# Kernel tuning notes

Measured on AMD Instinct MI355X. Metric: run time of the kernel, lower is better.

The kernel has to match this reference:

```python
import jax, jax.numpy as jnp
import numpy as np

GROUP_SIZE = 64
IN_FEATURES = 4096
OUT_FEATURES = 4096
NUM_GROUPS = OUT_FEATURES * IN_FEATURES // GROUP_SIZE  # 262144
BYTES_PER_GROUP = GROUP_SIZE // 8 * 3  # 24
TOKENS = 8192


def block_dequantize_3bit(packed, scale, group_size=GROUP_SIZE):
    # packed: (G, bytes_per_group) int32 holding byte values 0..255
    p = packed.astype(jnp.uint8).astype(jnp.int32)  # byte semantics
    t = p.reshape(p.shape[0], -1, 3)  # (G, group_size//8, 3)
    b0, b1, b2 = t[..., 0], t[..., 1], t[..., 2]
    c0 = b0 & 7
    c1 = (b0 >> 3) & 7
    c2 = ((b0 >> 6) & 3) | ((b1 & 1) << 2)
    c3 = (b1 >> 1) & 7
    c4 = (b1 >> 4) & 7
    c5 = ((b1 >> 7) & 1) | ((b2 & 3) << 1)
    c6 = (b2 >> 2) & 7
    c7 = (b2 >> 5) & 7
    codes = jnp.stack([c0, c1, c2, c3, c4, c5, c6, c7], axis=-1)
    codes = codes.reshape(p.shape[0], group_size)  # (G, group_size)
    q = jnp.clip(codes - 3, -3, 3).astype(jnp.float32)
    return (q * scale.astype(jnp.float32)).reshape(-1)


def setup_inputs() -> dict:
    key = jax.random.key(0)
    k1, k2, k3, k4 = jax.random.split(key, 4)
    x = jax.random.normal(k1, (TOKENS, IN_FEATURES), dtype=jnp.float32)
    weight_q3 = jax.random.randint(k2, (NUM_GROUPS, BYTES_PER_GROUP), 0, 256, dtype=jnp.int32)
    weight_scale = jax.random.uniform(k3, (NUM_GROUPS, 1), dtype=jnp.float32)
    bias = jax.random.normal(k4, (OUT_FEATURES,), dtype=jnp.float32)
    return {"x": x, "weight_q3": weight_q3, "weight_scale": weight_scale, "bias": bias}


def reference(x, weight_q3, weight_scale, bias):
    w = block_dequantize_3bit(weight_q3, weight_scale).reshape(OUT_FEATURES, IN_FEATURES)
    out = jnp.einsum('ti,oi->to', x.astype(jnp.float32), w) + bias
    return out.astype(x.dtype)
```

## Files before the change

kernel.cpp:

```cpp
#include <hip/hip_runtime.h>

#define M_TOK 8192
#define N_OUT 4096
#define K_IN  4096
#define BK    64
#define NT    (K_IN / BK)

typedef __bf16 bf16;
typedef bf16  bf16x4  __attribute__((ext_vector_type(4)));
typedef bf16  bf16x8  __attribute__((ext_vector_type(8)));
typedef float floatx4 __attribute__((ext_vector_type(4)));

__device__ __forceinline__ bf16 dec_code(int c, float s) {
    int q = (c > 6 ? 6 : c) - 3;
    return (bf16)((float)q * s);
}

__device__ __forceinline__ void async_ld16(const bf16* g, const bf16* l) {
    __builtin_amdgcn_global_load_lds(
        (const __attribute__((address_space(1))) void*)g,
        (__attribute__((address_space(3))) void*)l,
        16, 0, 0);
}

__global__ __launch_bounds__(256)
void dequant_kernel(const int* __restrict__ wq, const float* __restrict__ wscale,
                    bf16* __restrict__ W)
{
    int idx  = blockIdx.x * 256 + threadIdx.x;
    int g    = idx >> 1;
    int half = idx & 1;
    const int* wp = wq + (size_t)g * 24 + half * 12;
    int4 r0 = *(const int4*)(wp);
    int4 r1 = *(const int4*)(wp + 4);
    int4 r2 = *(const int4*)(wp + 8);
    float s = wscale[g];
    int by[12] = { r0.x, r0.y, r0.z, r0.w, r1.x, r1.y, r1.z, r1.w,
                   r2.x, r2.y, r2.z, r2.w };
    bf16* dst = W + (size_t)g * 64 + half * 32;
#pragma unroll
    for (int tri = 0; tri < 4; ++tri) {
        int b0 = by[tri * 3 + 0];
        int b1 = by[tri * 3 + 1];
        int b2 = by[tri * 3 + 2];
        bf16x8 h;
        h[0] = dec_code(b0 & 7, s);
        h[1] = dec_code((b0 >> 3) & 7, s);
        h[2] = dec_code(((b0 >> 6) & 3) | ((b1 & 1) << 2), s);
        h[3] = dec_code((b1 >> 1) & 7, s);
        h[4] = dec_code((b1 >> 4) & 7, s);
        h[5] = dec_code(((b1 >> 7) & 1) | ((b2 & 3) << 1), s);
        h[6] = dec_code((b2 >> 2) & 7, s);
        h[7] = dec_code((b2 >> 5) & 7, s);
        *(bf16x8*)(dst + tri * 8) = h;
    }
}

__global__ __launch_bounds__(256)
void cvt_kernel(const float* __restrict__ x, bf16* __restrict__ xb)
{
    size_t i = ((size_t)blockIdx.x * 256 + threadIdx.x) * 8;
    float4 a = *(const float4*)(x + i);
    float4 b = *(const float4*)(x + i + 4);
    bf16x8 h = { (bf16)a.x, (bf16)a.y, (bf16)a.z, (bf16)a.w,
                 (bf16)b.x, (bf16)b.y, (bf16)b.z, (bf16)b.w };
    *(bf16x8*)(xb + i) = h;
}

__global__ __launch_bounds__(256, 2)
void gemm_kernel(const bf16* __restrict__ A, const bf16* __restrict__ B,
                 const float* __restrict__ bias, float* __restrict__ out)
{
    __shared__ bf16 As[128][BK];
    __shared__ bf16 Bs[128][BK];

    const int t     = threadIdx.x;
    const int nBase = blockIdx.x * 128;
    const int mBase = blockIdx.y * 128;

    const int wave = t >> 6;
    const int lane = t & 63;
    const int quad = lane >> 4;
    const int r16  = lane & 15;
    const int wm   = wave & 1;
    const int wn   = wave >> 1;

    const int rr  = lane >> 3;
    const int cc  = lane & 7;
    const int lch = cc ^ rr;

    const bf16* aBase = A + (size_t)(mBase + wave * 32 + rr) * K_IN + lch * 8;
    const bf16* bBase = B + (size_t)(nBase + wave * 32 + rr) * K_IN + lch * 8;
    const bf16* aLds  = &As[wave * 32][0] + lane * 8;
    const bf16* bLds  = &Bs[wave * 32][0] + lane * 8;

    floatx4 acc[4][4];
#pragma unroll
    for (int i = 0; i < 4; ++i)
#pragma unroll
        for (int j = 0; j < 4; ++j)
            acc[i][j] = (floatx4){0.f, 0.f, 0.f, 0.f};

    const int sw = r16 & 7;

    for (int kt = 0; kt < NT; ++kt) {
        __syncthreads();
#pragma unroll
        for (int j = 0; j < 4; ++j) {
            async_ld16(aBase + (size_t)j * 8 * K_IN + kt * BK, aLds + j * 8 * BK);
            async_ld16(bBase + (size_t)j * 8 * K_IN + kt * BK, bLds + j * 8 * BK);
        }
        __syncthreads();

#pragma unroll
        for (int ks = 0; ks < 2; ++ks) {
            bf16x8 af[4], bfr[4];
#pragma unroll
            for (int mi = 0; mi < 4; ++mi)
                af[mi] = *(const bf16x8*)(&As[wm * 64 + mi * 16 + r16]
                                            [((ks * 4 + quad) ^ sw) * 8]);
#pragma unroll
            for (int ni = 0; ni < 4; ++ni)
                bfr[ni] = *(const bf16x8*)(&Bs[wn * 64 + ni * 16 + r16]
                                             [((ks * 4 + quad) ^ sw) * 8]);
#pragma unroll
            for (int mi = 0; mi < 4; ++mi)
#pragma unroll
                for (int ni = 0; ni < 4; ++ni)
                    acc[mi][ni] = __builtin_amdgcn_mfma_f32_16x16x32_bf16(
                        af[mi], bfr[ni], acc[mi][ni], 0, 0, 0);
        }
    }

    const int colBase = nBase + wn * 64;
#pragma unroll
    for (int ni = 0; ni < 4; ++ni) {
        int col  = colBase + ni * 16 + r16;
        float bv = bias[col];
#pragma unroll
        for (int mi = 0; mi < 4; ++mi) {
            int row0 = mBase + wm * 64 + mi * 16 + quad * 4;
#pragma unroll
            for (int r = 0; r < 4; ++r)
                out[(size_t)(row0 + r) * N_OUT + col] = acc[mi][ni][r] + bv;
        }
    }
}

__global__ __launch_bounds__(256, 2)
void linear3bit_fused(const float* __restrict__ x,
                      const int*   __restrict__ wq,
                      const float* __restrict__ wscale,
                      const float* __restrict__ bias,
                      float*       __restrict__ out)
{
    __shared__ bf16 As[128][BK];
    __shared__ bf16 Bs[128][BK];

    const int t     = threadIdx.x;
    const int mBase = blockIdx.y * 128;
    const int nBase = blockIdx.x * 128;

    const int wave = t >> 6;
    const int lane = t & 63;
    const int quad = lane >> 4;
    const int r16  = lane & 15;
    const int wm   = wave & 1;
    const int wn   = wave >> 1;

    floatx4 acc[4][4];
#pragma unroll
    for (int i = 0; i < 4; ++i)
#pragma unroll
        for (int j = 0; j < 4; ++j)
            acc[i][j] = (floatx4){0.f, 0.f, 0.f, 0.f};

    const int gl   = t >> 1;
    const int half = t & 1;
    const float* xBase = x + (size_t)mBase * K_IN;

    float4 aReg[8];
    int4   bReg[3];
    float  sReg;

    auto loadTile = [&](int kt) {
#pragma unroll
        for (int i = 0; i < 8; ++i) {
            int linear = i * 256 + t;
            int row    = linear >> 4;
            int c4     = (linear & 15) << 2;
            aReg[i] = *(const float4*)(xBase + (size_t)row * K_IN + kt * BK + c4);
        }
        size_t g = (size_t)(nBase + gl) * 64 + kt;
        const int* wp = wq + g * 24 + half * 12;
        bReg[0] = *(const int4*)(wp);
        bReg[1] = *(const int4*)(wp + 4);
        bReg[2] = *(const int4*)(wp + 8);
        sReg = wscale[g];
    };

    auto stage = [&]() {
#pragma unroll
        for (int i = 0; i < 8; ++i) {
            int linear = i * 256 + t;
            int row    = linear >> 4;
            int c4     = (linear & 15) << 2;
            float4 v = aReg[i];
            bf16x4 h = { (bf16)v.x, (bf16)v.y, (bf16)v.z, (bf16)v.w };
            *(bf16x4*)(&As[row][c4]) = h;
        }
        const float s = sReg;
        int by[12] = { bReg[0].x, bReg[0].y, bReg[0].z, bReg[0].w,
                       bReg[1].x, bReg[1].y, bReg[1].z, bReg[1].w,
                       bReg[2].x, bReg[2].y, bReg[2].z, bReg[2].w };
#pragma unroll
        for (int tri = 0; tri < 4; ++tri) {
            int b0 = by[tri * 3 + 0];
            int b1 = by[tri * 3 + 1];
            int b2 = by[tri * 3 + 2];
            bf16x8 h;
            h[0] = dec_code(b0 & 7, s);
            h[1] = dec_code((b0 >> 3) & 7, s);
            h[2] = dec_code(((b0 >> 6) & 3) | ((b1 & 1) << 2), s);
            h[3] = dec_code((b1 >> 1) & 7, s);
            h[4] = dec_code((b1 >> 4) & 7, s);
            h[5] = dec_code(((b1 >> 7) & 1) | ((b2 & 3) << 1), s);
            h[6] = dec_code((b2 >> 2) & 7, s);
            h[7] = dec_code((b2 >> 5) & 7, s);
            *(bf16x8*)(&Bs[gl][half * 32 + tri * 8]) = h;
        }
    };

    auto compute = [&]() {
#pragma unroll
        for (int ks = 0; ks < 2; ++ks) {
            bf16x8 af[4], bfr[4];
#pragma unroll
            for (int mi = 0; mi < 4; ++mi)
                af[mi] = *(const bf16x8*)(&As[wm * 64 + mi * 16 + r16][ks * 32 + quad * 8]);
#pragma unroll
            for (int ni = 0; ni < 4; ++ni)
                bfr[ni] = *(const bf16x8*)(&Bs[wn * 64 + ni * 16 + r16][ks * 32 + quad * 8]);
#pragma unroll
            for (int mi = 0; mi < 4; ++mi)
#pragma unroll
                for (int ni = 0; ni < 4; ++ni)
                    acc[mi][ni] = __builtin_amdgcn_mfma_f32_16x16x32_bf16(
                        af[mi], bfr[ni], acc[mi][ni], 0, 0, 0);
        }
    };

    loadTile(0);
    for (int kt = 0; kt < NT; ++kt) {
        __syncthreads();
        stage();
        __syncthreads();
        if (kt + 1 < NT) loadTile(kt + 1);
        compute();
    }

    const int colBase = nBase + wn * 64;
#pragma unroll
    for (int ni = 0; ni < 4; ++ni) {
        int col  = colBase + ni * 16 + r16;
        float bv = bias[col];
#pragma unroll
        for (int mi = 0; mi < 4; ++mi) {
            int row0 = mBase + wm * 64 + mi * 16 + quad * 4;
#pragma unroll
            for (int r = 0; r < 4; ++r)
                out[(size_t)(row0 + r) * N_OUT + col] = acc[mi][ni][r] + bv;
        }
    }
}

extern "C" void kernel_launch(void* const* d_in, const int* in_sizes, int n_in,
                              void* d_out, int out_size, void* d_ws, size_t ws_size,
                              hipStream_t stream) {
    const float* x      = (const float*)d_in[0];
    const int*   wq     = (const int*)d_in[1];
    const float* wscale = (const float*)d_in[2];
    const float* bias   = (const float*)d_in[3];
    float*       out    = (float*)d_out;

    const size_t wBytes  = (size_t)N_OUT * K_IN * sizeof(bf16);
    const size_t xBytes  = (size_t)M_TOK * K_IN * sizeof(bf16);

    if (ws_size >= wBytes + xBytes) {
        bf16* Wb = (bf16*)d_ws;
        bf16* Xb = (bf16*)((char*)d_ws + wBytes);
        dequant_kernel<<<2048, 256, 0, stream>>>(wq, wscale, Wb);
        cvt_kernel<<<16384, 256, 0, stream>>>(x, Xb);
        dim3 grid(N_OUT / 128, M_TOK / 128);
        gemm_kernel<<<grid, dim3(256), 0, stream>>>(Xb, Wb, bias, out);
    } else {
        dim3 grid(N_OUT / 128, M_TOK / 128);
        linear3bit_fused<<<grid, dim3(256), 0, stream>>>(x, wq, wscale, bias, out);
    }
}
```

Baseline: 484.5 us.

## Pre-swizzle dequantized weights into MFMA fragment order and load B directly to registers

The dequant kernel now writes weights in a layout that matches the MFMA B-fragment order, so each lane of the GEMM can fetch its B operand with a contiguous 16-byte global load. The B tile no longer goes through LDS, and the next k-tile is prefetched into registers while the current one is consumed. The aim is to cut LDS traffic and occupancy pressure for B. In exchange, each wave fetches its B fragments from global or L2 separately, with no sharing through LDS, and register pressure rises from the doubled B buffers. The cvt kernel also handles 16 elements per thread.

```diff
diff --git a/kernel.cpp b/kernel.cpp
--- a/kernel.cpp
+++ b/kernel.cpp
@@ -25,11 +25,16 @@
 
 __global__ __launch_bounds__(256)
 void dequant_kernel(const int* __restrict__ wq, const float* __restrict__ wscale,
-                    bf16* __restrict__ W)
+                    bf16* __restrict__ Wsw)
 {
     int idx  = blockIdx.x * 256 + threadIdx.x;
     int g    = idx >> 1;
     int half = idx & 1;
+    int n    = g >> 6;
+    int kg   = g & 63;
+    int k0   = kg * 2 + half;
+    int n0   = n >> 4;
+    int r16  = n & 15;
     const int* wp = wq + (size_t)g * 24 + half * 12;
     int4 r0 = *(const int4*)(wp);
     int4 r1 = *(const int4*)(wp + 4);
@@ -37,7 +42,7 @@
     float s = wscale[g];
     int by[12] = { r0.x, r0.y, r0.z, r0.w, r1.x, r1.y, r1.z, r1.w,
                    r2.x, r2.y, r2.z, r2.w };
-    bf16* dst = W + (size_t)g * 64 + half * 32;
+    bf16* dst = Wsw + (((size_t)n0 * 128 + k0) * 64 + r16) * 8;
 #pragma unroll
     for (int tri = 0; tri < 4; ++tri) {
         int b0 = by[tri * 3 + 0];
@@ -52,27 +57,29 @@
         h[5] = dec_code(((b1 >> 7) & 1) | ((b2 & 3) << 1), s);
         h[6] = dec_code((b2 >> 2) & 7, s);
         h[7] = dec_code((b2 >> 5) & 7, s);
-        *(bf16x8*)(dst + tri * 8) = h;
+        *(bf16x8*)(dst + (size_t)tri * 16 * 8) = h;
     }
 }
 
 __global__ __launch_bounds__(256)
 void cvt_kernel(const float* __restrict__ x, bf16* __restrict__ xb)
 {
-    size_t i = ((size_t)blockIdx.x * 256 + threadIdx.x) * 8;
-    float4 a = *(const float4*)(x + i);
-    float4 b = *(const float4*)(x + i + 4);
-    bf16x8 h = { (bf16)a.x, (bf16)a.y, (bf16)a.z, (bf16)a.w,
-                 (bf16)b.x, (bf16)b.y, (bf16)b.z, (bf16)b.w };
-    *(bf16x8*)(xb + i) = h;
+    size_t i = ((size_t)blockIdx.x * 256 + threadIdx.x) * 16;
+#pragma unroll
+    for (int h = 0; h < 2; ++h) {
+        float4 a = *(const float4*)(x + i + h * 8);
+        float4 b = *(const float4*)(x + i + h * 8 + 4);
+        bf16x8 v = { (bf16)a.x, (bf16)a.y, (bf16)a.z, (bf16)a.w,
+                     (bf16)b.x, (bf16)b.y, (bf16)b.z, (bf16)b.w };
+        *(bf16x8*)(xb + i + h * 8) = v;
+    }
 }
 
 __global__ __launch_bounds__(256, 2)
-void gemm_kernel(const bf16* __restrict__ A, const bf16* __restrict__ B,
+void gemm_kernel(const bf16* __restrict__ A, const bf16* __restrict__ Wsw,
                  const float* __restrict__ bias, float* __restrict__ out)
 {
     __shared__ bf16 As[128][BK];
-    __shared__ bf16 Bs[128][BK];
 
     const int t     = threadIdx.x;
     const int nBase = blockIdx.x * 128;
@@ -88,11 +95,10 @@
     const int rr  = lane >> 3;
     const int cc  = lane & 7;
     const int lch = cc ^ rr;
-
     const bf16* aBase = A + (size_t)(mBase + wave * 32 + rr) * K_IN + lch * 8;
-    const bf16* bBase = B + (size_t)(nBase + wave * 32 + rr) * K_IN + lch * 8;
     const bf16* aLds  = &As[wave * 32][0] + lane * 8;
-    const bf16* bLds  = &Bs[wave * 32][0] + lane * 8;
+
+    const bf16* bBase = Wsw + (((size_t)(nBase >> 4) + wn * 4) * 128 * 64 + lane) * 8;
 
     floatx4 acc[4][4];
 #pragma unroll
@@ -103,33 +109,47 @@
 
     const int sw = r16 & 7;
 
+    bf16x8 bcur[2][4], bnxt[2][4];
+#pragma unroll
+    for (int ks = 0; ks < 2; ++ks)
+#pragma unroll
+        for (int ni = 0; ni < 4; ++ni)
+            bcur[ks][ni] = *(const bf16x8*)(bBase + ((size_t)ni * 128 + ks) * 512);
+
     for (int kt = 0; kt < NT; ++kt) {
         __syncthreads();
 #pragma unroll
-        for (int j = 0; j < 4; ++j) {
+        for (int j = 0; j < 4; ++j)
             async_ld16(aBase + (size_t)j * 8 * K_IN + kt * BK, aLds + j * 8 * BK);
-            async_ld16(bBase + (size_t)j * 8 * K_IN + kt * BK, bLds + j * 8 * BK);
+        if (kt + 1 < NT) {
+#pragma unroll
+            for (int ks = 0; ks < 2; ++ks)
+#pragma unroll
+                for (int ni = 0; ni < 4; ++ni)
+                    bnxt[ks][ni] = *(const bf16x8*)(
+                        bBase + ((size_t)ni * 128 + (kt + 1) * 2 + ks) * 512);
         }
         __syncthreads();
 
 #pragma unroll
         for (int ks = 0; ks < 2; ++ks) {
-            bf16x8 af[4], bfr[4];
+            bf16x8 af[4];
 #pragma unroll
             for (int mi = 0; mi < 4; ++mi)
                 af[mi] = *(const bf16x8*)(&As[wm * 64 + mi * 16 + r16]
                                             [((ks * 4 + quad) ^ sw) * 8]);
 #pragma unroll
-            for (int ni = 0; ni < 4; ++ni)
-                bfr[ni] = *(const bf16x8*)(&Bs[wn * 64 + ni * 16 + r16]
-                                             [((ks * 4 + quad) ^ sw) * 8]);
-#pragma unroll
             for (int mi = 0; mi < 4; ++mi)
 #pragma unroll
                 for (int ni = 0; ni < 4; ++ni)
                     acc[mi][ni] = __builtin_amdgcn_mfma_f32_16x16x32_bf16(
-                        af[mi], bfr[ni], acc[mi][ni], 0, 0, 0);
-        }
+                        af[mi], bcur[ks][ni], acc[mi][ni], 0, 0, 0);
+        }
+#pragma unroll
+        for (int ks = 0; ks < 2; ++ks)
+#pragma unroll
+            for (int ni = 0; ni < 4; ++ni)
+                bcur[ks][ni] = bnxt[ks][ni];
     }
 
     const int colBase = nBase + wn * 64;
@@ -290,7 +310,7 @@
         bf16* Wb = (bf16*)d_ws;
         bf16* Xb = (bf16*)((char*)d_ws + wBytes);
         dequant_kernel<<<2048, 256, 0, stream>>>(wq, wscale, Wb);
-        cvt_kernel<<<16384, 256, 0, stream>>>(x, Xb);
+        cvt_kernel<<<8192, 256, 0, stream>>>(x, Xb);
         dim3 grid(N_OUT / 128, M_TOK / 128);
         gemm_kernel<<<grid, dim3(256), 0, stream>>>(Xb, Wb, bias, out);
     } else {
```

Measured after the change: 513.1 us. 5.9% more time.
